# Performance work log

Hardware: AMD Instinct MI355X
Metric: run time of the kernel (lower is better)

The kernel has to match this reference:

```python
import jax, jax.numpy as jnp
import numpy as np

RADIUS = 0.1
NSAMPLE = 64


def ball_query(xyz, new_xyz, pointsnum, radius, nsample):
    """xyz (B,N,2), new_xyz (B,S,2), pointsnum (B,) -> idx (B,S,nsample) int32.
    Mirrors CUDA ball_query: for each query take the first `nsample` point
    indices (in index order) whose squared distance < radius^2 and index <
    pointsnum[b]; slots beyond the number found are padded with the first
    found index (0 if none found)."""
    N = xyz.shape[1]
    # (B,S,N) squared distances
    d2 = jnp.sum((new_xyz[:, :, None, :] - xyz[:, None, :, :]) ** 2, axis=-1)
    valid = jnp.arange(N, dtype=jnp.int32)[None, None, :] < pointsnum[:, None, None]
    mask = (d2 < radius * radius) & valid
    # key = point index if in ball else N (sentinel); smallest `nsample` keys
    key = jnp.where(mask, jnp.arange(N, dtype=jnp.int32), N)
    neg_small, _ = jax.lax.top_k(-key, nsample)          # largest of -key == smallest keys
    sorted_keys = -neg_small                              # ascending in-ball indices, N-padded
    first = sorted_keys[..., :1]
    pad = jnp.where(first < N, first, 0)
    idx = jnp.where(sorted_keys < N, sorted_keys, pad)
    return idx.astype(jnp.int32)


def group(features, idx):
    """features (B,C,N), idx (B,S,K) -> (B,C,S,K)."""
    return jax.vmap(lambda f, i: f[:, i])(features, idx)


def setup_inputs() -> dict:
    key = jax.random.key(0)
    k1, k2, k3 = jax.random.split(key, 3)
    B, N, S, C = 4, 16384, 2048, 64
    xyz = jax.random.uniform(k1, (B, N, 2), dtype=jnp.float32)
    new_xyz = jax.random.uniform(k2, (B, S, 2), dtype=jnp.float32)
    features = jax.random.normal(k3, (B, C, N), dtype=jnp.float32)
    pointsnum = jnp.full((B,), N, dtype=jnp.int32)
    return {"xyz": xyz, "new_xyz": new_xyz, "features": features, "pointsnum": pointsnum}


def reference(xyz, new_xyz, features, pointsnum):
    # QueryAndGroup(radius=RADIUS, nsample=NSAMPLE, use_xyz=True)
    idx = ball_query(xyz, new_xyz, pointsnum, RADIUS, NSAMPLE)  # (B,S,K) int32
    xyz_t = jnp.transpose(xyz, (0, 2, 1))                        # (B,2,N)
    grouped_xyz = group(xyz_t, idx)                              # (B,2,S,K)
    grouped_xyz = grouped_xyz - jnp.transpose(new_xyz, (0, 2, 1))[..., None]
    grouped_features = group(features, idx)                      # (B,C,S,K)
    new_features = jnp.concatenate([grouped_xyz, grouped_features], axis=1)  # (B,2+C,S,K)
    return new_features
```

## Files before the change

kernel.cpp:

```cpp
#include <hip/hip_runtime.h>
#include <stdint.h>

#define B 4
#define N 16384
#define S 2048
#define C 64
#define K 64
#define OC 66
#define R2 0.01f
#define NXCD 8
#define TP 1089

typedef float f32x4 __attribute__((ext_vector_type(4)));

__global__ __launch_bounds__(256) void transpose_kernel(const float* __restrict__ f,
                                                        float* __restrict__ ft) {
    __shared__ float tile[64 * 65];
    const int n0 = blockIdx.x * 64;
    const int b  = blockIdx.y;
    const int t  = threadIdx.x;

    const int nl = t & 63, cl = t >> 6;
    #pragma unroll
    for (int cc = cl; cc < 64; cc += 4) {
        tile[cc * 65 + nl] = __builtin_nontemporal_load(&f[((size_t)b * C + cc) * N + n0 + nl]);
    }
    __syncthreads();

    const int cl2 = t & 63, nl2 = t >> 6;
    #pragma unroll
    for (int nn = nl2; nn < 64; nn += 4) {
        ft[((size_t)b * N + n0 + nn) * C + cl2] = tile[cl2 * 65 + nn];
    }
}

__global__ __launch_bounds__(256) void qag3_kernel(const float* __restrict__ xyz,
                                                   const float* __restrict__ new_xyz,
                                                   const float* __restrict__ ft,
                                                   const int* __restrict__ pointsnum,
                                                   float* __restrict__ out) {
    __shared__ int   s_idx[4][K];
    __shared__ float tile[4 * TP];

    const int t    = threadIdx.x;
    const int lane = t & 63;
    const int wu   = __builtin_amdgcn_readfirstlane(t >> 6);

    const int nwg = (B * S) / 4;
    const int bid = blockIdx.x;
    const int swz = (bid & (NXCD - 1)) * (nwg / NXCD) + (bid >> 3);

    const int q0 = swz * 4;
    const int b  = q0 >> 11;
    const int q  = q0 + wu;
    const int s  = (q0 & (S - 1)) + wu;

    const float qx = new_xyz[(size_t)q * 2 + 0];
    const float qy = new_xyz[(size_t)q * 2 + 1];
    const float* __restrict__ xb = xyz + (size_t)b * N * 2;

    int pn = pointsnum[b];
    pn = pn < 0 ? 0 : (pn > N ? N : pn);
    int cnt = 0;
    float2 p[4], pf[4];
    #pragma unroll
    for (int u = 0; u < 4; ++u) {
        const int i  = u * 64 + lane;
        const int ic = i < N ? i : N - 1;
        p[u] = *(const float2*)&xb[(size_t)ic * 2];
    }
    for (int base = 0; base < pn && cnt < K; base += 256) {
        #pragma unroll
        for (int u = 0; u < 4; ++u) {
            const int i  = base + 256 + u * 64 + lane;
            const int ic = i < N ? i : N - 1;
            pf[u] = *(const float2*)&xb[(size_t)ic * 2];
        }
        #pragma unroll
        for (int u = 0; u < 4; ++u) {
            const int i = base + u * 64 + lane;
            bool ok = false;
            if (i < pn) {
                const float dx = __fsub_rn(qx, p[u].x);
                const float dy = __fsub_rn(qy, p[u].y);
                const float d2 = __fadd_rn(__fmul_rn(dx, dx), __fmul_rn(dy, dy));
                ok = d2 < R2;
            }
            const unsigned long long m = __ballot(ok);
            if (ok) {
                const int pos = cnt + __popcll(m & ((1ull << lane) - 1ull));
                if (pos < K) s_idx[wu][pos] = i;
            }
            cnt += __popcll(m);
        }
        #pragma unroll
        for (int u = 0; u < 4; ++u) p[u] = pf[u];
    }
    const int found = cnt < K ? cnt : K;
    const int first = (found > 0) ? s_idx[wu][0] : 0;
    const int id    = (lane < found) ? s_idx[wu][lane] : first;
    s_idx[wu][lane] = id;

    const size_t SK = (size_t)S * K;
    const float2 pxy = *(const float2*)&xb[(size_t)id * 2];
    float* ob = out + ((size_t)b * OC) * SK + (size_t)s * K;
    ob[lane]      = pxy.x - qx;
    ob[SK + lane] = pxy.y - qy;

    const int kk = lane >> 2;
    const int c2 = lane & 3;
    const float* __restrict__ ftb = ft + (size_t)b * N * C;
    float* owt = tile + wu * TP;

    #pragma unroll
    for (int cc = 0; cc < 4; ++cc) {
        f32x4 v[4];
        #pragma unroll
        for (int g = 0; g < 4; ++g) {
            const int pt = g * 16 + kk;
            const int ip = s_idx[wu][pt];
            v[g] = *(const f32x4*)&ftb[(size_t)ip * C + cc * 16 + c2 * 4];
        }
        #pragma unroll
        for (int g = 0; g < 4; ++g) {
            const int pt = g * 16 + kk;
            *(f32x4*)&owt[pt * 17 + c2 * 4] = v[g];
        }
        #pragma unroll
        for (int c = 0; c < 16; ++c) {
            const float vv = owt[lane * 17 + c];
            ob[(size_t)(2 + cc * 16 + c) * SK + lane] = vv;
        }
    }
}

__global__ __launch_bounds__(256) void qag_fallback(const float* __restrict__ xyz,
                                                    const float* __restrict__ new_xyz,
                                                    const float* __restrict__ feat,
                                                    const int* __restrict__ pointsnum,
                                                    float* __restrict__ out) {
    __shared__ int s_idx[4][K];

    const int t    = threadIdx.x;
    const int lane = t & 63;
    const int wu   = __builtin_amdgcn_readfirstlane(t >> 6);
    const int q0   = blockIdx.x * 4;
    const int b    = q0 >> 11;
    const int q    = q0 + wu;
    const int s    = (q0 & (S - 1)) + wu;

    const float qx = new_xyz[(size_t)q * 2 + 0];
    const float qy = new_xyz[(size_t)q * 2 + 1];
    const float* __restrict__ xb = xyz + (size_t)b * N * 2;

    int pn = pointsnum[b];
    pn = pn < 0 ? 0 : (pn > N ? N : pn);
    int cnt = 0;
    for (int base = 0; base < pn && cnt < K; base += 256) {
        float2 p[4];
        #pragma unroll
        for (int u = 0; u < 4; ++u) {
            int i  = base + u * 64 + lane;
            int ic = i < N ? i : N - 1;
            p[u] = *(const float2*)&xb[(size_t)ic * 2];
        }
        #pragma unroll
        for (int u = 0; u < 4; ++u) {
            const int i = base + u * 64 + lane;
            bool ok = false;
            if (i < pn) {
                const float dx = __fsub_rn(qx, p[u].x);
                const float dy = __fsub_rn(qy, p[u].y);
                const float d2 = __fadd_rn(__fmul_rn(dx, dx), __fmul_rn(dy, dy));
                ok = d2 < R2;
            }
            const unsigned long long mm = __ballot(ok);
            if (ok) {
                const int pos = cnt + __popcll(mm & ((1ull << lane) - 1ull));
                if (pos < K) s_idx[wu][pos] = i;
            }
            cnt += __popcll(mm);
        }
    }
    const int found = cnt < K ? cnt : K;
    const int first = (found > 0) ? s_idx[wu][0] : 0;
    const int id    = (lane < found) ? s_idx[wu][lane] : first;

    const size_t SK = (size_t)S * K;
    const float2 pxy = *(const float2*)&xb[(size_t)id * 2];
    float* ob = out + ((size_t)b * OC) * SK + (size_t)s * K;
    ob[lane]      = pxy.x - qx;
    ob[SK + lane] = pxy.y - qy;

    const float* __restrict__ fb = feat + (size_t)b * C * N;
    for (int c = 0; c < C; ++c) {
        ob[(size_t)(2 + c) * SK + lane] = fb[(size_t)c * N + id];
    }
}

extern "C" void kernel_launch(void* const* d_in, const int* in_sizes, int n_in,
                              void* d_out, int out_size, void* d_ws, size_t ws_size,
                              hipStream_t stream) {
    const float* xyz       = (const float*)d_in[0];
    const float* new_xyz   = (const float*)d_in[1];
    const float* feat      = (const float*)d_in[2];
    const int*   pointsnum = (const int*)d_in[3];
    float*       out       = (float*)d_out;

    const size_t ft_bytes = (size_t)B * N * C * sizeof(float);
    if (ws_size >= ft_bytes) {
        float* ft = (float*)d_ws;
        transpose_kernel<<<dim3(N / 64, B), 256, 0, stream>>>(feat, ft);
        qag3_kernel<<<B * S / 4, 256, 0, stream>>>(xyz, new_xyz, ft, pointsnum, out);
    } else {
        qag_fallback<<<B * S / 4, 256, 0, stream>>>(xyz, new_xyz, feat, pointsnum, out);
    }
}
```

Measured before the change: 48.66 us.

## Overlap transpose with ball query in one launch, split gather into separate kernel

```diff
diff --git a/kernel.cpp b/kernel.cpp
--- a/kernel.cpp
+++ b/kernel.cpp
@@ -9,51 +9,46 @@
 #define OC 66
 #define R2 0.01f
 #define NXCD 8
-#define TP 1089
 
 typedef float f32x4 __attribute__((ext_vector_type(4)));
 
-__global__ __launch_bounds__(256) void transpose_kernel(const float* __restrict__ f,
-                                                        float* __restrict__ ft) {
+__global__ __launch_bounds__(256) void prep_kernel(const float* __restrict__ f,
+                                                   const float* __restrict__ xyz,
+                                                   const float* __restrict__ new_xyz,
+                                                   const int* __restrict__ pointsnum,
+                                                   float* __restrict__ ft,
+                                                   int* __restrict__ idx,
+                                                   float* __restrict__ out) {
     __shared__ float tile[64 * 65];
-    const int n0 = blockIdx.x * 64;
-    const int b  = blockIdx.y;
-    const int t  = threadIdx.x;
-
-    const int nl = t & 63, cl = t >> 6;
-    #pragma unroll
-    for (int cc = cl; cc < 64; cc += 4) {
-        tile[cc * 65 + nl] = __builtin_nontemporal_load(&f[((size_t)b * C + cc) * N + n0 + nl]);
-    }
-    __syncthreads();
-
-    const int cl2 = t & 63, nl2 = t >> 6;
-    #pragma unroll
-    for (int nn = nl2; nn < 64; nn += 4) {
-        ft[((size_t)b * N + n0 + nn) * C + cl2] = tile[cl2 * 65 + nn];
-    }
-}
-
-__global__ __launch_bounds__(256) void qag3_kernel(const float* __restrict__ xyz,
-                                                   const float* __restrict__ new_xyz,
-                                                   const float* __restrict__ ft,
-                                                   const int* __restrict__ pointsnum,
-                                                   float* __restrict__ out) {
     __shared__ int   s_idx[4][K];
-    __shared__ float tile[4 * TP];
-
-    const int t    = threadIdx.x;
+
+    const int t = threadIdx.x;
+
+    if (blockIdx.x < 1024) {
+        const int n0 = (blockIdx.x & 255) * 64;
+        const int b  = blockIdx.x >> 8;
+
+        const int nl = t & 63, cl = t >> 6;
+        #pragma unroll
+        for (int cc = cl; cc < 64; cc += 4) {
+            tile[cc * 65 + nl] = __builtin_nontemporal_load(&f[((size_t)b * C + cc) * N + n0 + nl]);
+        }
+        __syncthreads();
+
+        const int cl2 = t & 63, nl2 = t >> 6;
+        #pragma unroll
+        for (int nn = nl2; nn < 64; nn += 4) {
+            ft[((size_t)b * N + n0 + nn) * C + cl2] = tile[cl2 * 65 + nn];
+        }
+        return;
+    }
+
     const int lane = t & 63;
     const int wu   = __builtin_amdgcn_readfirstlane(t >> 6);
-
-    const int nwg = (B * S) / 4;
-    const int bid = blockIdx.x;
-    const int swz = (bid & (NXCD - 1)) * (nwg / NXCD) + (bid >> 3);
-
-    const int q0 = swz * 4;
-    const int b  = q0 >> 11;
-    const int q  = q0 + wu;
-    const int s  = (q0 & (S - 1)) + wu;
+    const int q0   = (int)(blockIdx.x - 1024) * 4;
+    const int b    = q0 >> 11;
+    const int q    = q0 + wu;
+    const int s    = (q0 & (S - 1)) + wu;
 
     const float qx = new_xyz[(size_t)q * 2 + 0];
     const float qy = new_xyz[(size_t)q * 2 + 1];
@@ -99,37 +94,56 @@
     const int found = cnt < K ? cnt : K;
     const int first = (found > 0) ? s_idx[wu][0] : 0;
     const int id    = (lane < found) ? s_idx[wu][lane] : first;
-    s_idx[wu][lane] = id;
+
+    idx[(size_t)q * K + lane] = id;
 
     const size_t SK = (size_t)S * K;
     const float2 pxy = *(const float2*)&xb[(size_t)id * 2];
     float* ob = out + ((size_t)b * OC) * SK + (size_t)s * K;
     ob[lane]      = pxy.x - qx;
     ob[SK + lane] = pxy.y - qy;
+}
+
+__global__ __launch_bounds__(256) void gather2_kernel(const float* __restrict__ ft,
+                                                      const int* __restrict__ idx,
+                                                      float* __restrict__ out) {
+    const int t    = threadIdx.x;
+    const int lane = t & 63;
+    const int wu   = __builtin_amdgcn_readfirstlane(t >> 6);
+
+    const int nwg = (B * S) / 4;
+    const int bid = blockIdx.x;
+    const int swz = (bid & (NXCD - 1)) * (nwg / NXCD) + (bid >> 3);
+
+    const int q0 = swz * 4;
+    const int b  = q0 >> 11;
+    const int q  = q0 + wu;
+    const int s  = (q0 & (S - 1)) + wu;
 
     const int kk = lane >> 2;
     const int c2 = lane & 3;
+
+    int ids[4];
+    #pragma unroll
+    for (int g = 0; g < 4; ++g) {
+        ids[g] = idx[(size_t)q * K + g * 16 + kk];
+    }
+
     const float* __restrict__ ftb = ft + (size_t)b * N * C;
-    float* owt = tile + wu * TP;
+    const size_t SK = (size_t)S * K;
+    float* ob = out + ((size_t)b * OC) * SK + (size_t)s * K;
 
     #pragma unroll
     for (int cc = 0; cc < 4; ++cc) {
-        f32x4 v[4];
         #pragma unroll
         for (int g = 0; g < 4; ++g) {
-            const int pt = g * 16 + kk;
-            const int ip = s_idx[wu][pt];
-            v[g] = *(const f32x4*)&ftb[(size_t)ip * C + cc * 16 + c2 * 4];
-        }
-        #pragma unroll
-        for (int g = 0; g < 4; ++g) {
-            const int pt = g * 16 + kk;
-            *(f32x4*)&owt[pt * 17 + c2 * 4] = v[g];
-        }
-        #pragma unroll
-        for (int c = 0; c < 16; ++c) {
-            const float vv = owt[lane * 17 + c];
-            ob[(size_t)(2 + cc * 16 + c) * SK + lane] = vv;
+            const f32x4 v = *(const f32x4*)&ftb[(size_t)ids[g] * C + cc * 16 + c2 * 4];
+            const int k = g * 16 + kk;
+            const int c = 2 + cc * 16 + c2 * 4;
+            ob[(size_t)(c + 0) * SK + k] = v.x;
+            ob[(size_t)(c + 1) * SK + k] = v.y;
+            ob[(size_t)(c + 2) * SK + k] = v.z;
+            ob[(size_t)(c + 3) * SK + k] = v.w;
         }
     }
 }
@@ -207,11 +221,14 @@
     const int*   pointsnum = (const int*)d_in[3];
     float*       out       = (float*)d_out;
 
-    const size_t ft_bytes = (size_t)B * N * C * sizeof(float);
-    if (ws_size >= ft_bytes) {
-        float* ft = (float*)d_ws;
-        transpose_kernel<<<dim3(N / 64, B), 256, 0, stream>>>(feat, ft);
-        qag3_kernel<<<B * S / 4, 256, 0, stream>>>(xyz, new_xyz, ft, pointsnum, out);
+    const size_t ft_bytes  = (size_t)B * N * C * sizeof(float);
+    const size_t idx_bytes = (size_t)B * S * K * sizeof(int);
+
+    if (ws_size >= ft_bytes + idx_bytes) {
+        float* ft  = (float*)d_ws;
+        int*   idx = (int*)((char*)d_ws + ft_bytes);
+        prep_kernel<<<1024 + B * S / 4, 256, 0, stream>>>(feat, xyz, new_xyz, pointsnum, ft, idx, out);
+        gather2_kernel<<<B * S / 4, 256, 0, stream>>>(ft, idx, out);
     } else {
         qag_fallback<<<B * S / 4, 256, 0, stream>>>(xyz, new_xyz, feat, pointsnum, out);
     }
```

Measured after the change: 54.37 us. 11.7% more time.
